# Performance work log

Measured on AMD Instinct MI355X. Metric: run time of the kernel, lower is better.

## Reference

```python
import jax, jax.numpy as jnp
import numpy as np

B, S, D, H = 2, 2048, 512, 8
DK = D // H
MASK_VALUE = -1e9


def setup_inputs() -> dict:
    key = jax.random.key(0)
    ks = jax.random.split(key, 12)
    scale = 1.0 / np.sqrt(D)
    inp = {
        "query": jax.random.normal(ks[0], (B, S, D), jnp.float32),
        "key": jax.random.normal(ks[1], (B, S, D), jnp.float32),
        "value": jax.random.normal(ks[2], (B, S, D), jnp.float32),
        # causal mask, broadcastable over batch and heads
        "mask": jnp.tril(jnp.ones((S, S), jnp.int32))[None, None, :, :],
        "Wq": jax.random.normal(ks[3], (D, D), jnp.float32) * scale,
        "bq": jax.random.normal(ks[4], (D,), jnp.float32) * scale,
        "Wk": jax.random.normal(ks[5], (D, D), jnp.float32) * scale,
        "bk": jax.random.normal(ks[6], (D,), jnp.float32) * scale,
        "Wv": jax.random.normal(ks[7], (D, D), jnp.float32) * scale,
        "bv": jax.random.normal(ks[8], (D,), jnp.float32) * scale,
        "Wo": jax.random.normal(ks[9], (D, D), jnp.float32) * scale,
        "bo": jax.random.normal(ks[10], (D,), jnp.float32) * scale,
    }
    return inp


def reference(query, key, value, mask, Wq, bq, Wk, bk, Wv, bv, Wo, bo):
    # linear projections (torch Linear: x @ W.T + b)
    q = query @ Wq.T + bq
    k = key @ Wk.T + bk
    v = value @ Wv.T + bv
    # split heads: [B,S,D] -> [B,H,S,DK]
    q = q.reshape(B, S, H, DK).transpose(0, 2, 1, 3)
    k = k.reshape(B, S, H, DK).transpose(0, 2, 1, 3)
    v = v.reshape(B, S, H, DK).transpose(0, 2, 1, 3)
    # scaled dot-product attention with explicit [B,H,S,S] score matrix
    scores = jnp.einsum("bhqd,bhkd->bhqk", q, k) / jnp.sqrt(jnp.float32(DK))
    scores = jnp.where(mask == 0, jnp.float32(MASK_VALUE), scores)
    attn = jax.nn.softmax(scores, axis=-1)
    x = jnp.einsum("bhqk,bhkd->bhqd", attn, v)
    # merge heads: [B,H,S,DK] -> [B,S,D]
    x = x.transpose(0, 2, 1, 3).reshape(B, S, D)
    return x @ Wo.T + bo
```

## Files before the change

### kernel.cpp

```cpp
#include <hip/hip_runtime.h>
#include <hip/hip_bf16.h>

#define B_   2
#define S_   2048
#define D_   512
#define H_   8
#define DK_  64
#define M_   (B_*S_)

typedef float  floatx4 __attribute__((ext_vector_type(4)));
typedef __bf16 bf16x8  __attribute__((ext_vector_type(8)));

#define MFMA16x16x32(a,b,c) __builtin_amdgcn_mfma_f32_16x16x32_bf16((a),(b),(c),0,0,0)

static __device__ __forceinline__ void load_lds16(const void* g, void* l) {
  __builtin_amdgcn_global_load_lds(
      (const __attribute__((address_space(1))) void*)g,
      (__attribute__((address_space(3))) void*)l,
      16, 0, 0);
}

__global__ __launch_bounds__(256) void cvt_inputs(
    const float* __restrict__ w0, const float* __restrict__ w1,
    const float* __restrict__ w2, const float* __restrict__ w3,
    const float* __restrict__ x0, const float* __restrict__ x1,
    const float* __restrict__ x2,
    __bf16* __restrict__ out)
{
  const int idx = (blockIdx.x * 256 + threadIdx.x) * 4;
  const float* src;
  int off;
  if (idx < 1048576) {
    src = (idx < 524288) ? ((idx < 262144) ? w0 : w1)
                         : ((idx < 786432) ? w2 : w3);
    off = idx & 0x3FFFF;
  } else {
    const int i2 = idx - 1048576;
    const int xs = i2 >> 21;
    src = (xs == 0) ? x0 : (xs == 1) ? x1 : x2;
    off = i2 & 0x1FFFFF;
  }
  float4 v = *(const float4*)(src + off);
  __bf16* o = out + idx;
  o[0]=(__bf16)v.x; o[1]=(__bf16)v.y; o[2]=(__bf16)v.z; o[3]=(__bf16)v.w;
}


__global__ __launch_bounds__(256) void proj_qkv(
    const __bf16* __restrict__ Xb, const __bf16* __restrict__ Wball,
    const float* __restrict__ bq, const float* __restrict__ bk, const float* __restrict__ bv,
    __bf16* __restrict__ Qb, __bf16* __restrict__ Kb, __bf16* __restrict__ Vtb)
{
  __shared__ __align__(16) __bf16 smem[16384];

  const int z = blockIdx.z;
  const __bf16* X    = Xb + (size_t)z * (M_*D_);
  const __bf16* W    = Wball + (size_t)z * (D_*D_);
  const float*  bias = (z==0) ? bq : (z==1) ? bk : bv;

  const int m0 = blockIdx.x * 128;
  const int n0 = blockIdx.y * 128;
  const int tid  = threadIdx.x;
  const int w    = tid >> 6;
  const int lane = tid & 63;
  const int lcol = lane & 15;
  const int quad = lane >> 4;
  const int wm = w >> 1, wn = w & 1;

  floatx4 zero = {0.f,0.f,0.f,0.f};
  floatx4 acc[4][4];
#pragma unroll
  for (int i = 0; i < 4; ++i)
#pragma unroll
    for (int nt = 0; nt < 4; ++nt) acc[i][nt] = zero;

  auto stage = [&](int bsel, int k0) {
#pragma unroll
    for (int j = 0; j < 2; ++j) {
      const int u0 = (j*4 + w) * 64;
      const int u  = u0 + lane;
      const int row = u >> 2, c16 = (u & 3) * 8;
      load_lds16(X + (size_t)(m0 + row)*D_ + k0 + c16,
                 (char*)(smem + bsel*4096) + u0*16);
      load_lds16(W + (size_t)(n0 + row)*D_ + k0 + c16,
                 (char*)(smem + 8192 + bsel*4096) + u0*16);
    }
  };

  stage(0, 0);
  for (int it = 0; it < 16; ++it) {
    __syncthreads();
    if (it + 1 < 16) stage((it+1)&1, (it+1)*32);
    const __bf16* ab = smem + (it&1)*4096;
    const __bf16* bb = smem + 8192 + (it&1)*4096;
    bf16x8 af[4], bf[4];
#pragma unroll
    for (int i = 0; i < 4; ++i)
      af[i] = *(const bf16x8*)(ab + (wm*64 + i*16 + lcol)*32 + quad*8);
#pragma unroll
    for (int nt = 0; nt < 4; ++nt)
      bf[nt] = *(const bf16x8*)(bb + (wn*64 + nt*16 + lcol)*32 + quad*8);
#pragma unroll
    for (int i = 0; i < 4; ++i)
#pragma unroll
      for (int nt = 0; nt < 4; ++nt)
        acc[i][nt] = MFMA16x16x32(af[i], bf[nt], acc[i][nt]);
  }

  __syncthreads();
#pragma unroll
  for (int nt = 0; nt < 4; ++nt) {
    const int n = n0 + wn*64 + nt*16 + lcol;
    const float bias_n = bias[n];
    const int h_l = (n >> 6) & 1;
    const int dk  = n & 63;
#pragma unroll
    for (int i = 0; i < 4; ++i)
#pragma unroll
      for (int r = 0; r < 4; ++r) {
        const int m = m0 + wm*64 + i*16 + quad*4 + r;
        const float val = acc[i][nt][r] + bias_n;
        const int p = h_l*2 + ((m >> 6) & 1);
        const int klo = m & 63;
        int off;
        if (z == 0) {
          off = klo*64 + dk;
        } else if (z == 1) {
          off = (((klo>>4)*2 + (dk>>5))*64 + ((dk>>3)&3)*16 + (klo&15))*8 + (dk&7);
        } else {
          off = (((dk>>4)*2 + (klo>>5))*64 + ((klo>>3)&3)*16 + (dk&15))*8 + (klo&7);
        }
        smem[p*4096 + off] = (__bf16)val;
      }
  }
  __syncthreads();

  __bf16* dst = (z==0) ? Qb : (z==1) ? Kb : Vtb;
  const int bb2  = m0 >> 11;
  const int hh0  = n0 >> 6;
  const int cc0  = (m0 & 2047) >> 6;
#pragma unroll
  for (int it2 = 0; it2 < 8; ++it2) {
    const int u = it2*256 + tid;
    const int p = u >> 9, o = u & 511;
    const size_t base = ((size_t)(bb2*H_ + hh0 + (p>>1)))*(S_*DK_)
                      + (size_t)(cc0 + (p&1))*4096;
    *(bf16x8*)(dst + base + o*8) = *(const bf16x8*)(smem + p*4096 + o*8);
  }
}

__global__ __launch_bounds__(128) void attn_fwd(
    const __bf16* __restrict__ Qb, const __bf16* __restrict__ Kb,
    const __bf16* __restrict__ Vtb, __bf16* __restrict__ attnb)
{
  __shared__ __align__(16) __bf16 kbuf[2][4096];
  __shared__ __align__(16) __bf16 vbuf[2][4096];
  __shared__ __align__(16) __bf16 pbuf[2][16*72];

  const int tid  = threadIdx.x;
  const int w    = tid >> 6;
  const int lane = tid & 63;
  const int lcol = lane & 15;
  const int quad = lane >> 4;
  const int hh = blockIdx.y;
  const int bb = blockIdx.z;

  const int t   = 63 - blockIdx.x;
  const int q0  = t * 32;
  const int qr0 = q0 + w*16;

  const __bf16* Qp = Qb  + (size_t)(bb*H_ + hh) * S_ * DK_;
  const __bf16* Kp = Kb  + (size_t)(bb*H_ + hh) * S_ * DK_;
  const __bf16* Vp = Vtb + (size_t)(bb*H_ + hh) * DK_ * S_;

  const bf16x8 aq0 = *(const bf16x8*)(Qp + (size_t)(qr0 + lcol)*DK_ + quad*8);
  const bf16x8 aq1 = *(const bf16x8*)(Qp + (size_t)(qr0 + lcol)*DK_ + 32 + quad*8);

  floatx4 zero = {0.f,0.f,0.f,0.f};
  floatx4 acc[4] = {zero, zero, zero, zero};
  float lsum[4] = {0.f, 0.f, 0.f, 0.f};

  auto stage_chunk = [&](int bsel, int c) {
    const char* ksrc = (const char*)(Kp + (size_t)c * 4096);
    const char* vsrc = (const char*)(Vp + (size_t)c * 4096);
#pragma unroll
    for (int j = 0; j < 4; ++j) {
      const int off = (j*2 + w) * 1024;
      load_lds16(ksrc + off + lane*16, (char*)kbuf[bsel] + off);
      load_lds16(vsrc + off + lane*16, (char*)vbuf[bsel] + off);
    }
  };

  const int nch = (t + 2) >> 1;
  stage_chunk(0, 0);
  for (int c = 0; c < nch; ++c) {
    __syncthreads();
    if (c + 1 < nch) stage_chunk((c+1)&1, c+1);
    const int bsel = c & 1;
    const int k0 = c * 64;
    const __bf16* kb = kbuf[bsel];
    const __bf16* vb = vbuf[bsel];

    floatx4 s[4];
#pragma unroll
    for (int nt = 0; nt < 4; ++nt) {
      bf16x8 kf0 = *(const bf16x8*)(kb + (nt*2+0)*512 + lane*8);
      bf16x8 kf1 = *(const bf16x8*)(kb + (nt*2+1)*512 + lane*8);
      s[nt] = MFMA16x16x32(aq1, kf1, MFMA16x16x32(aq0, kf0, zero));
    }

    const bool edge = (k0 + 63 > qr0);
#pragma unroll
    for (int nt = 0; nt < 4; ++nt) {
#pragma unroll
      for (int r = 0; r < 4; ++r) {
        float p = __expf(s[nt][r] * 0.125f);
        if (edge) {
          const int qrow = qr0 + quad*4 + r;
          if (k0 + nt*16 + lcol > qrow) p = 0.f;
        }
        lsum[r] += p;
        pbuf[w][(quad*4 + r)*72 + nt*16 + lcol] = (__bf16)p;
      }
    }
    asm volatile("s_waitcnt lgkmcnt(0)" ::: "memory");

    const bf16x8 pa0 = *(const bf16x8*)(&pbuf[w][lcol*72 + quad*8]);
    const bf16x8 pa1 = *(const bf16x8*)(&pbuf[w][lcol*72 + 32 + quad*8]);
#pragma unroll
    for (int nt = 0; nt < 4; ++nt) {
      bf16x8 vf0 = *(const bf16x8*)(vb + (nt*2+0)*512 + lane*8);
      bf16x8 vf1 = *(const bf16x8*)(vb + (nt*2+1)*512 + lane*8);
      acc[nt] = MFMA16x16x32(pa0, vf0, acc[nt]);
      acc[nt] = MFMA16x16x32(pa1, vf1, acc[nt]);
    }
  }

  float rinv[4];
#pragma unroll
  for (int r = 0; r < 4; ++r) {
    float tv = lsum[r];
    tv += __shfl_xor(tv, 1, 16);
    tv += __shfl_xor(tv, 2, 16);
    tv += __shfl_xor(tv, 4, 16);
    tv += __shfl_xor(tv, 8, 16);
    rinv[r] = 1.0f / tv;
  }

#pragma unroll
  for (int nt = 0; nt < 4; ++nt)
#pragma unroll
    for (int r = 0; r < 4; ++r) {
      const int q = qr0 + quad*4 + r;
      attnb[((size_t)(bb*S_ + q)) * D_ + hh*DK_ + nt*16 + lcol] =
          (__bf16)(acc[nt][r] * rinv[r]);
    }
}

__global__ __launch_bounds__(256) void proj_out(
    const __bf16* __restrict__ attnb, const __bf16* __restrict__ Wob,
    const float* __restrict__ bo, float* __restrict__ out)
{
  __shared__ __align__(16) __bf16 abuf[2][128*32];
  __shared__ __align__(16) __bf16 bbuf[2][128*32];

  const int m0 = blockIdx.x * 128;
  const int n0 = blockIdx.y * 128;
  const int tid  = threadIdx.x;
  const int w    = tid >> 6;
  const int lane = tid & 63;
  const int lcol = lane & 15;
  const int quad = lane >> 4;
  const int wm = w >> 1, wn = w & 1;

  floatx4 zero = {0.f,0.f,0.f,0.f};
  floatx4 acc[4][4];
#pragma unroll
  for (int i = 0; i < 4; ++i)
#pragma unroll
    for (int nt = 0; nt < 4; ++nt) acc[i][nt] = zero;

  auto stage = [&](int bsel, int k0) {
#pragma unroll
    for (int j = 0; j < 2; ++j) {
      const int u0 = (j*4 + w) * 64;
      const int u  = u0 + lane;
      const int row = u >> 2, c16 = (u & 3) * 8;
      load_lds16(attnb + (size_t)(m0 + row)*D_ + k0 + c16,
                 (char*)&abuf[bsel][0] + u0*16);
      load_lds16(Wob + (size_t)(n0 + row)*D_ + k0 + c16,
                 (char*)&bbuf[bsel][0] + u0*16);
    }
  };

  stage(0, 0);
  for (int it = 0; it < 16; ++it) {
    __syncthreads();
    if (it + 1 < 16) stage((it+1)&1, (it+1)*32);
    const __bf16* ab = &abuf[it&1][0];
    const __bf16* bb = &bbuf[it&1][0];
    bf16x8 af[4], bf[4];
#pragma unroll
    for (int i = 0; i < 4; ++i)
      af[i] = *(const bf16x8*)(ab + (wm*64 + i*16 + lcol)*32 + quad*8);
#pragma unroll
    for (int nt = 0; nt < 4; ++nt)
      bf[nt] = *(const bf16x8*)(bb + (wn*64 + nt*16 + lcol)*32 + quad*8);
#pragma unroll
    for (int i = 0; i < 4; ++i)
#pragma unroll
      for (int nt = 0; nt < 4; ++nt)
        acc[i][nt] = MFMA16x16x32(af[i], bf[nt], acc[i][nt]);
  }

#pragma unroll
  for (int nt = 0; nt < 4; ++nt) {
    const int n = n0 + wn*64 + nt*16 + lcol;
    const float bias_n = bo[n];
#pragma unroll
    for (int i = 0; i < 4; ++i)
#pragma unroll
      for (int r = 0; r < 4; ++r) {
        const int m = m0 + wm*64 + i*16 + quad*4 + r;
        out[(size_t)m * D_ + n] = acc[i][nt][r] + bias_n;
      }
  }
}

extern "C" void kernel_launch(void* const* d_in, const int* in_sizes, int n_in,
                              void* d_out, int out_size, void* d_ws, size_t ws_size,
                              hipStream_t stream) {
  const float* q_in = (const float*)d_in[0];
  const float* k_in = (const float*)d_in[1];
  const float* v_in = (const float*)d_in[2];
  const float* Wq = (const float*)d_in[4];
  const float* bq = (const float*)d_in[5];
  const float* Wk = (const float*)d_in[6];
  const float* bk = (const float*)d_in[7];
  const float* Wv = (const float*)d_in[8];
  const float* bv = (const float*)d_in[9];
  const float* Wo = (const float*)d_in[10];
  const float* bo = (const float*)d_in[11];
  float* out = (float*)d_out;

  __bf16* ws    = (__bf16*)d_ws;
  __bf16* Qb    = ws;
  __bf16* Kb    = ws + 1*2097152;
  __bf16* Vtb   = ws + 2*2097152;
  __bf16* attnb = ws + 3*2097152;
  __bf16* Wb    = ws + 4*2097152;
  __bf16* Xb    = Wb + 4*262144;

  cvt_inputs<<<dim3(7168), dim3(256), 0, stream>>>(
      Wq, Wk, Wv, Wo, q_in, k_in, v_in, Wb);

  proj_qkv<<<dim3(M_/128, D_/128, 3), dim3(256), 0, stream>>>(
      Xb, Wb, bq, bk, bv, Qb, Kb, Vtb);

  attn_fwd<<<dim3(64, H_, B_), dim3(128), 0, stream>>>(Qb, Kb, Vtb, attnb);

  proj_out<<<dim3(M_/128, D_/128), dim3(256), 0, stream>>>(
      attnb, Wb + 3*262144, bo, out);
}
```

Measured before the change: 176.0 us.

## Shrink GEMM tiles and make attention waves independent with register double-buffered K/V

Measured after the change: 189.7 us. 1.08x slower.

```diff
diff --git a/kernel.cpp b/kernel.cpp
--- a/kernel.cpp
+++ b/kernel.cpp
@@ -51,39 +51,40 @@
     const float* __restrict__ bq, const float* __restrict__ bk, const float* __restrict__ bv,
     __bf16* __restrict__ Qb, __bf16* __restrict__ Kb, __bf16* __restrict__ Vtb)
 {
-  __shared__ __align__(16) __bf16 smem[16384];
+  __shared__ __align__(16) __bf16 smem[12288];
 
   const int z = blockIdx.z;
   const __bf16* X    = Xb + (size_t)z * (M_*D_);
   const __bf16* W    = Wball + (size_t)z * (D_*D_);
   const float*  bias = (z==0) ? bq : (z==1) ? bk : bv;
 
-  const int m0 = blockIdx.x * 128;
+  const int m0 = blockIdx.x * 64;
   const int n0 = blockIdx.y * 128;
   const int tid  = threadIdx.x;
   const int w    = tid >> 6;
   const int lane = tid & 63;
   const int lcol = lane & 15;
   const int quad = lane >> 4;
-  const int wm = w >> 1, wn = w & 1;
+  const int wm = w & 1, wn = w >> 1;
 
   floatx4 zero = {0.f,0.f,0.f,0.f};
-  floatx4 acc[4][4];
-#pragma unroll
-  for (int i = 0; i < 4; ++i)
+  floatx4 acc[2][4];
+#pragma unroll
+  for (int i = 0; i < 2; ++i)
 #pragma unroll
     for (int nt = 0; nt < 4; ++nt) acc[i][nt] = zero;
 
   auto stage = [&](int bsel, int k0) {
+    {
+      const int u = w*64 + lane;
+      load_lds16(X + (size_t)(m0 + (u >> 2))*D_ + k0 + (u & 3)*8,
+                 (char*)(smem + bsel*2048) + w*1024);
+    }
 #pragma unroll
     for (int j = 0; j < 2; ++j) {
-      const int u0 = (j*4 + w) * 64;
-      const int u  = u0 + lane;
-      const int row = u >> 2, c16 = (u & 3) * 8;
-      load_lds16(X + (size_t)(m0 + row)*D_ + k0 + c16,
-                 (char*)(smem + bsel*4096) + u0*16);
-      load_lds16(W + (size_t)(n0 + row)*D_ + k0 + c16,
-                 (char*)(smem + 8192 + bsel*4096) + u0*16);
+      const int u = (j*4 + w)*64 + lane;
+      load_lds16(W + (size_t)(n0 + (u >> 2))*D_ + k0 + (u & 3)*8,
+                 (char*)(smem + 4096 + bsel*4096) + (j*4 + w)*1024);
     }
   };
 
@@ -91,17 +92,17 @@
   for (int it = 0; it < 16; ++it) {
     __syncthreads();
     if (it + 1 < 16) stage((it+1)&1, (it+1)*32);
-    const __bf16* ab = smem + (it&1)*4096;
-    const __bf16* bb = smem + 8192 + (it&1)*4096;
-    bf16x8 af[4], bf[4];
-#pragma unroll
-    for (int i = 0; i < 4; ++i)
-      af[i] = *(const bf16x8*)(ab + (wm*64 + i*16 + lcol)*32 + quad*8);
+    const __bf16* ab = smem + (it&1)*2048;
+    const __bf16* bb = smem + 4096 + (it&1)*4096;
+    bf16x8 af[2], bf[4];
+#pragma unroll
+    for (int i = 0; i < 2; ++i)
+      af[i] = *(const bf16x8*)(ab + (wm*32 + i*16 + lcol)*32 + quad*8);
 #pragma unroll
     for (int nt = 0; nt < 4; ++nt)
       bf[nt] = *(const bf16x8*)(bb + (wn*64 + nt*16 + lcol)*32 + quad*8);
 #pragma unroll
-    for (int i = 0; i < 4; ++i)
+    for (int i = 0; i < 2; ++i)
 #pragma unroll
       for (int nt = 0; nt < 4; ++nt)
         acc[i][nt] = MFMA16x16x32(af[i], bf[nt], acc[i][nt]);
@@ -115,12 +116,11 @@
     const int h_l = (n >> 6) & 1;
     const int dk  = n & 63;
 #pragma unroll
-    for (int i = 0; i < 4; ++i)
+    for (int i = 0; i < 2; ++i)
 #pragma unroll
       for (int r = 0; r < 4; ++r) {
-        const int m = m0 + wm*64 + i*16 + quad*4 + r;
+        const int m = m0 + wm*32 + i*16 + quad*4 + r;
         const float val = acc[i][nt][r] + bias_n;
-        const int p = h_l*2 + ((m >> 6) & 1);
         const int klo = m & 63;
         int off;
         if (z == 0) {
@@ -130,32 +130,29 @@
         } else {
           off = (((dk>>4)*2 + (klo>>5))*64 + ((klo>>3)&3)*16 + (dk&15))*8 + (klo&7);
         }
-        smem[p*4096 + off] = (__bf16)val;
+        smem[h_l*4096 + off] = (__bf16)val;
       }
   }
   __syncthreads();
 
   __bf16* dst = (z==0) ? Qb : (z==1) ? Kb : Vtb;
-  const int bb2  = m0 >> 11;
-  const int hh0  = n0 >> 6;
-  const int cc0  = (m0 & 2047) >> 6;
-#pragma unroll
-  for (int it2 = 0; it2 < 8; ++it2) {
+  const int bb2 = m0 >> 11;
+  const int hh0 = n0 >> 6;
+  const int cc0 = (m0 & 2047) >> 6;
+#pragma unroll
+  for (int it2 = 0; it2 < 4; ++it2) {
     const int u = it2*256 + tid;
     const int p = u >> 9, o = u & 511;
-    const size_t base = ((size_t)(bb2*H_ + hh0 + (p>>1)))*(S_*DK_)
-                      + (size_t)(cc0 + (p&1))*4096;
+    const size_t base = ((size_t)(bb2*H_ + hh0 + p))*(S_*DK_) + (size_t)cc0*4096;
     *(bf16x8*)(dst + base + o*8) = *(const bf16x8*)(smem + p*4096 + o*8);
   }
 }
 
-__global__ __launch_bounds__(128) void attn_fwd(
+__global__ __launch_bounds__(256, 2) void attn_fwd(
     const __bf16* __restrict__ Qb, const __bf16* __restrict__ Kb,
     const __bf16* __restrict__ Vtb, __bf16* __restrict__ attnb)
 {
-  __shared__ __align__(16) __bf16 kbuf[2][4096];
-  __shared__ __align__(16) __bf16 vbuf[2][4096];
-  __shared__ __align__(16) __bf16 pbuf[2][16*72];
+  __shared__ __align__(16) __bf16 pbuf[4][16*72];
 
   const int tid  = threadIdx.x;
   const int w    = tid >> 6;
@@ -165,9 +162,8 @@
   const int hh = blockIdx.y;
   const int bb = blockIdx.z;
 
-  const int t   = 63 - blockIdx.x;
-  const int q0  = t * 32;
-  const int qr0 = q0 + w*16;
+  const int t   = 127 - (blockIdx.x*4 + w);
+  const int qr0 = t * 16;
 
   const __bf16* Qp = Qb  + (size_t)(bb*H_ + hh) * S_ * DK_;
   const __bf16* Kp = Kb  + (size_t)(bb*H_ + hh) * S_ * DK_;
@@ -180,41 +176,28 @@
   floatx4 acc[4] = {zero, zero, zero, zero};
   float lsum[4] = {0.f, 0.f, 0.f, 0.f};
 
-  auto stage_chunk = [&](int bsel, int c) {
-    const char* ksrc = (const char*)(Kp + (size_t)c * 4096);
-    const char* vsrc = (const char*)(Vp + (size_t)c * 4096);
-#pragma unroll
-    for (int j = 0; j < 4; ++j) {
-      const int off = (j*2 + w) * 1024;
-      load_lds16(ksrc + off + lane*16, (char*)kbuf[bsel] + off);
-      load_lds16(vsrc + off + lane*16, (char*)vbuf[bsel] + off);
-    }
+  bf16x8 kA[8], vA[8], kB[8], vB[8];
+
+  auto ld = [&](bf16x8 (&kf)[8], bf16x8 (&vf)[8], int c) {
+    const __bf16* kp = Kp + (size_t)c*4096 + lane*8;
+    const __bf16* vp = Vp + (size_t)c*4096 + lane*8;
+#pragma unroll
+    for (int i = 0; i < 8; ++i) kf[i] = *(const bf16x8*)(kp + i*512);
+#pragma unroll
+    for (int i = 0; i < 8; ++i) vf[i] = *(const bf16x8*)(vp + i*512);
   };
 
-  const int nch = (t + 2) >> 1;
-  stage_chunk(0, 0);
-  for (int c = 0; c < nch; ++c) {
-    __syncthreads();
-    if (c + 1 < nch) stage_chunk((c+1)&1, c+1);
-    const int bsel = c & 1;
-    const int k0 = c * 64;
-    const __bf16* kb = kbuf[bsel];
-    const __bf16* vb = vbuf[bsel];
-
+  auto compute = [&](const bf16x8 (&kc)[8], const bf16x8 (&vc)[8],
+                     int k0, bool edge) {
     floatx4 s[4];
 #pragma unroll
+    for (int nt = 0; nt < 4; ++nt)
+      s[nt] = MFMA16x16x32(aq1, kc[nt*2+1], MFMA16x16x32(aq0, kc[nt*2+0], zero));
+#pragma unroll
     for (int nt = 0; nt < 4; ++nt) {
-      bf16x8 kf0 = *(const bf16x8*)(kb + (nt*2+0)*512 + lane*8);
-      bf16x8 kf1 = *(const bf16x8*)(kb + (nt*2+1)*512 + lane*8);
-      s[nt] = MFMA16x16x32(aq1, kf1, MFMA16x16x32(aq0, kf0, zero));
-    }
-
-    const bool edge = (k0 + 63 > qr0);
-#pragma unroll
-    for (int nt = 0; nt < 4; ++nt) {
 #pragma unroll
       for (int r = 0; r < 4; ++r) {
-        float p = __expf(s[nt][r] * 0.125f);
+        float p = exp2f(s[nt][r] * 0.18033688011112042f);
         if (edge) {
           const int qrow = qr0 + quad*4 + r;
           if (k0 + nt*16 + lcol > qrow) p = 0.f;
@@ -224,17 +207,23 @@
       }
     }
     asm volatile("s_waitcnt lgkmcnt(0)" ::: "memory");
-
     const bf16x8 pa0 = *(const bf16x8*)(&pbuf[w][lcol*72 + quad*8]);
     const bf16x8 pa1 = *(const bf16x8*)(&pbuf[w][lcol*72 + 32 + quad*8]);
 #pragma unroll
     for (int nt = 0; nt < 4; ++nt) {
-      bf16x8 vf0 = *(const bf16x8*)(vb + (nt*2+0)*512 + lane*8);
-      bf16x8 vf1 = *(const bf16x8*)(vb + (nt*2+1)*512 + lane*8);
-      acc[nt] = MFMA16x16x32(pa0, vf0, acc[nt]);
-      acc[nt] = MFMA16x16x32(pa1, vf1, acc[nt]);
-    }
-  }
+      acc[nt] = MFMA16x16x32(pa0, vc[nt*2+0], acc[nt]);
+      acc[nt] = MFMA16x16x32(pa1, vc[nt*2+1], acc[nt]);
+    }
+  };
+
+  const int nch = (t >> 2) + 1;
+  ld(kA, vA, 0);
+  for (int c = 0; c + 1 < nch; ++c) {
+    if (c & 1) { ld(kA, vA, c+1); compute(kB, vB, c*64, false); }
+    else       { ld(kB, vB, c+1); compute(kA, vA, c*64, false); }
+  }
+  if ((nch - 1) & 1) compute(kB, vB, (nch-1)*64, true);
+  else               compute(kA, vA, (nch-1)*64, true);
 
   float rinv[4];
 #pragma unroll
@@ -261,35 +250,35 @@
     const __bf16* __restrict__ attnb, const __bf16* __restrict__ Wob,
     const float* __restrict__ bo, float* __restrict__ out)
 {
-  __shared__ __align__(16) __bf16 abuf[2][128*32];
-  __shared__ __align__(16) __bf16 bbuf[2][128*32];
-
-  const int m0 = blockIdx.x * 128;
+  __shared__ __align__(16) __bf16 smem[12288];
+
+  const int m0 = blockIdx.x * 64;
   const int n0 = blockIdx.y * 128;
   const int tid  = threadIdx.x;
   const int w    = tid >> 6;
   const int lane = tid & 63;
   const int lcol = lane & 15;
   const int quad = lane >> 4;
-  const int wm = w >> 1, wn = w & 1;
+  const int wm = w & 1, wn = w >> 1;
 
   floatx4 zero = {0.f,0.f,0.f,0.f};
-  floatx4 acc[4][4];
-#pragma unroll
-  for (int i = 0; i < 4; ++i)
+  floatx4 acc[2][4];
+#pragma unroll
+  for (int i = 0; i < 2; ++i)
 #pragma unroll
     for (int nt = 0; nt < 4; ++nt) acc[i][nt] = zero;
 
   auto stage = [&](int bsel, int k0) {
+    {
+      const int u = w*64 + lane;
+      load_lds16(attnb + (size_t)(m0 + (u >> 2))*D_ + k0 + (u & 3)*8,
+                 (char*)(smem + bsel*2048) + w*1024);
+    }
 #pragma unroll
     for (int j = 0; j < 2; ++j) {
-      const int u0 = (j*4 + w) * 64;
-      const int u  = u0 + lane;
-      const int row = u >> 2, c16 = (u & 3) * 8;
-      load_lds16(attnb + (size_t)(m0 + row)*D_ + k0 + c16,
-                 (char*)&abuf[bsel][0] + u0*16);
-      load_lds16(Wob + (size_t)(n0 + row)*D_ + k0 + c16,
-                 (char*)&bbuf[bsel][0] + u0*16);
+      const int u = (j*4 + w)*64 + lane;
+      load_lds16(Wob + (size_t)(n0 + (u >> 2))*D_ + k0 + (u & 3)*8,
+                 (char*)(smem + 4096 + bsel*4096) + (j*4 + w)*1024);
     }
   };
 
@@ -297,17 +286,17 @@
   for (int it = 0; it < 16; ++it) {
     __syncthreads();
     if (it + 1 < 16) stage((it+1)&1, (it+1)*32);
-    const __bf16* ab = &abuf[it&1][0];
-    const __bf16* bb = &bbuf[it&1][0];
-    bf16x8 af[4], bf[4];
-#pragma unroll
-    for (int i = 0; i < 4; ++i)
-      af[i] = *(const bf16x8*)(ab + (wm*64 + i*16 + lcol)*32 + quad*8);
+    const __bf16* ab = smem + (it&1)*2048;
+    const __bf16* bb = smem + 4096 + (it&1)*4096;
+    bf16x8 af[2], bf[4];
+#pragma unroll
+    for (int i = 0; i < 2; ++i)
+      af[i] = *(const bf16x8*)(ab + (wm*32 + i*16 + lcol)*32 + quad*8);
 #pragma unroll
     for (int nt = 0; nt < 4; ++nt)
       bf[nt] = *(const bf16x8*)(bb + (wn*64 + nt*16 + lcol)*32 + quad*8);
 #pragma unroll
-    for (int i = 0; i < 4; ++i)
+    for (int i = 0; i < 2; ++i)
 #pragma unroll
       for (int nt = 0; nt < 4; ++nt)
         acc[i][nt] = MFMA16x16x32(af[i], bf[nt], acc[i][nt]);
@@ -318,10 +307,10 @@
     const int n = n0 + wn*64 + nt*16 + lcol;
     const float bias_n = bo[n];
 #pragma unroll
-    for (int i = 0; i < 4; ++i)
+    for (int i = 0; i < 2; ++i)
 #pragma unroll
       for (int r = 0; r < 4; ++r) {
-        const int m = m0 + wm*64 + i*16 + quad*4 + r;
+        const int m = m0 + wm*32 + i*16 + quad*4 + r;
         out[(size_t)m * D_ + n] = acc[i][nt][r] + bias_n;
       }
   }
@@ -354,11 +343,11 @@
   cvt_inputs<<<dim3(7168), dim3(256), 0, stream>>>(
       Wq, Wk, Wv, Wo, q_in, k_in, v_in, Wb);
 
-  proj_qkv<<<dim3(M_/128, D_/128, 3), dim3(256), 0, stream>>>(
+  proj_qkv<<<dim3(M_/64, D_/128, 3), dim3(256), 0, stream>>>(
       Xb, Wb, bq, bk, bv, Qb, Kb, Vtb);
 
-  attn_fwd<<<dim3(64, H_, B_), dim3(128), 0, stream>>>(Qb, Kb, Vtb, attnb);
-
-  proj_out<<<dim3(M_/128, D_/128), dim3(256), 0, stream>>>(
+  attn_fwd<<<dim3(32, H_, B_), dim3(256), 0, stream>>>(Qb, Kb, Vtb, attnb);
+
+  proj_out<<<dim3(M_/64, D_/128), dim3(256), 0, stream>>>(
       attnb, Wb + 3*262144, bo, out);
 }
```
